# Performance work log

Measured on AMD Instinct MI355X. Metric: run time of the kernel, lower is better.

## Reference

```python
import jax, jax.numpy as jnp
import numpy as np

D_MODEL, D_K, D_V, H = 1024, 64, 64, 16
B, NQ, NK = 4, 1024, 1024
HID = D_MODEL // 2


def _dwg(x, W1, b1, W2, b2):
    # DynamicWeightGenerator: sigmoid(fc2(relu(fc1(x))))
    h = jax.nn.relu(jnp.einsum('bnd,hd->bnh', x, W1) + b1)
    return jax.nn.sigmoid(jnp.einsum('bnh,dh->bnd', h, W2) + b2)


def setup_inputs() -> dict:
    key = jax.random.key(0)
    ks = jax.random.split(key, 32)
    s = 0.02
    inp = {
        'queries': jax.random.normal(ks[0], (B, NQ, D_MODEL), jnp.float32),
        'keys': jax.random.normal(ks[1], (B, NK, D_MODEL), jnp.float32),
        'values': jax.random.normal(ks[2], (B, NK, D_MODEL), jnp.float32),
        'attention_mask': jax.random.randint(ks[3], (B, 1, NQ, NK), 0, 2) > 0,
        'attention_weights': jax.random.uniform(ks[4], (B, H, NQ, NK), jnp.float32),
        'memory': jax.random.normal(ks[5], (B, NK), jnp.float32),
        # projections (torch Linear convention: y = x @ W.T + b)
        'Wq': jax.random.normal(ks[6], (H * D_K, D_MODEL), jnp.float32) * s,
        'bq': jnp.zeros((H * D_K,), jnp.float32),
        'Wk': jax.random.normal(ks[7], (H * D_K, D_MODEL), jnp.float32) * s,
        'bk': jnp.zeros((H * D_K,), jnp.float32),
        'Wv': jax.random.normal(ks[8], (H * D_V, D_MODEL), jnp.float32) * s,
        'bv': jnp.zeros((H * D_V,), jnp.float32),
        'Wo': jax.random.normal(ks[9], (D_MODEL, H * D_V), jnp.float32) * s,
        'bo': jnp.zeros((D_MODEL,), jnp.float32),
        'Wmm': jax.random.normal(ks[10], (H * D_V, 1), jnp.float32) * s,
        'bmm': jnp.zeros((H * D_V,), jnp.float32),
    }
    for i, tag in enumerate(['q', 'k', 'v']):
        k0, k1 = ks[11 + 2 * i], ks[12 + 2 * i]
        inp[f'W1{tag}'] = jax.random.normal(k0, (HID, D_MODEL), jnp.float32) * s
        inp[f'b1{tag}'] = jnp.zeros((HID,), jnp.float32)
        inp[f'W2{tag}'] = jax.random.normal(k1, (D_MODEL, HID), jnp.float32) * s
        inp[f'b2{tag}'] = jnp.zeros((D_MODEL,), jnp.float32)
    return inp


def reference(queries, keys, values, attention_mask, attention_weights, memory,
              Wq, bq, Wk, bk, Wv, bv, Wo, bo, Wmm, bmm,
              W1q, b1q, W2q, b2q, W1k, b1k, W2k, b2k, W1v, b1v, W2v, b2v):
    b_s, nq = queries.shape[:2]
    nk = keys.shape[1]
    # dynamic elementwise gating of inputs
    q_in = queries * _dwg(queries, W1q, b1q, W2q, b2q)
    k_in = keys * _dwg(keys, W1k, b1k, W2k, b2k)
    v_in = values * _dwg(values, W1v, b1v, W2v, b2v)
    # projections -> (b, h, n, d)
    q = (jnp.einsum('bnd,ed->bne', q_in, Wq) + bq).reshape(b_s, nq, H, D_K).transpose(0, 2, 1, 3)
    k = (jnp.einsum('bnd,ed->bne', k_in, Wk) + bk).reshape(b_s, nk, H, D_K).transpose(0, 2, 1, 3)
    v = (jnp.einsum('bnd,ed->bne', v_in, Wv) + bv).reshape(b_s, nk, H, D_V).transpose(0, 2, 1, 3)
    # per-token memory factor: fc_mm(memory[..., None]) -> (b, h, nk, d_k)
    mm = (memory[..., None] * Wmm[:, 0] + bmm).reshape(b_s, nk, H, D_K).transpose(0, 2, 1, 3)
    att = jnp.einsum('bhqd,bhkd->bhqk', q, k * mm) / np.sqrt(D_K).astype(np.float32)
    att = att * attention_weights                         # custom scaling (slice [:nk] == full)
    att = jnp.where(attention_mask, -jnp.inf, att)        # masked_fill
    att = jax.nn.softmax(att, axis=-1)
    out = jnp.einsum('bhqk,bhkd->bhqd', att, v * mm)      # (b, h, nq, d_v)
    out = out.transpose(0, 2, 1, 3).reshape(b_s, nq, H * D_V)
    return jnp.einsum('bne,de->bnd', out, Wo) + bo
```

## Files before the change

### kernel.cpp

```cpp
#include <hip/hip_runtime.h>
#include <hip/hip_bf16.h>

#define BB    4
#define NN    1024
#define DM    1024
#define HH    16
#define HID   512
#define TT    (BB * NN)

typedef __attribute__((ext_vector_type(8))) short bf16x8;
typedef __attribute__((ext_vector_type(4))) float f32x4;

__device__ __forceinline__ ushort f2bfu(float f) {
    __hip_bfloat16 h = __float2bfloat16(f);
    return __builtin_bit_cast(ushort, h);
}

__device__ __forceinline__ float bfu2f(ushort u) {
    __hip_bfloat16 h = __builtin_bit_cast(__hip_bfloat16, u);
    return __bfloat162float(h);
}

__device__ __forceinline__ f32x4 mfma16(bf16x8 a, bf16x8 b, f32x4 c) {
    return __builtin_amdgcn_mfma_f32_16x16x32_bf16(a, b, c, 0, 0, 0);
}

__device__ __forceinline__ void gll16(const void* g, void* l) {
    __builtin_amdgcn_global_load_lds(
        (const __attribute__((address_space(1))) unsigned int*)g,
        (__attribute__((address_space(3))) unsigned int*)l, 16, 0, 0);
}

__global__ void detect_mask_kernel(const uint4* __restrict__ m,
                                   int n16, int* __restrict__ flags) {
    int stride = blockDim.x * gridDim.x;
    unsigned hi = 0, lo = 0;
    for (int i = blockIdx.x * blockDim.x + threadIdx.x; i < n16; i += stride) {
        uint4 v = m[i];
        unsigned o = v.x | v.y | v.z | v.w;
        lo |= o & 0xFFu;
        hi |= o & 0xFFFFFF00u;
    }
    if (hi) atomicOr(&flags[0], 1);
    if (lo) atomicOr(&flags[1], 1);
}

#define NSEG 13
struct CvtAll { const float* s[NSEG]; ushort* d[NSEG]; int bound[NSEG]; };

__global__ __launch_bounds__(256) void cvt_all(CvtAll a, int total) {
    int stride = blockDim.x * gridDim.x;
    for (int i = blockIdx.x * blockDim.x + threadIdx.x; i < total; i += stride) {
        const float* sp = a.s[0];
        ushort* dp = a.d[0];
        int base = 0;
        #pragma unroll
        for (int k = 1; k < NSEG; ++k) {
            bool ge = i >= a.bound[k - 1];
            sp = ge ? a.s[k] : sp;
            dp = ge ? a.d[k] : dp;
            base = ge ? a.bound[k - 1] : base;
        }
        int j = i - base;
        float4 v = ((const float4*)sp)[j];
        uint2 o;
        o.x = (unsigned)f2bfu(v.x) | ((unsigned)f2bfu(v.y) << 16);
        o.y = (unsigned)f2bfu(v.z) | ((unsigned)f2bfu(v.w) << 16);
        ((uint2*)dp)[j] = o;
    }
}

struct GB {
    const ushort* A[3]; const ushort* W[3];
    const float* bias[3]; void* C[3]; const ushort* X[3];
};

template <int EP, int NF>
__global__ __launch_bounds__(256) void gemm_bf16(
    GB gb, int M, int N, int K,
    const float* __restrict__ mem, const float* __restrict__ Wmm,
    const float* __restrict__ bmm)
{
    __shared__ __align__(16) ushort As[2][128 * 64];
    __shared__ __align__(16) ushort Bs[2][NF * 32 * 64];
    const int z = blockIdx.z;
    const ushort* A = gb.A[z];
    const ushort* W = gb.W[z];
    const float* bias = gb.bias[z];
    void* Cout = gb.C[z];
    const ushort* X = gb.X[z];

    const int tid = threadIdx.x;
    const int lane = tid & 63, w = tid >> 6;
    const int lc = lane & 15, lg = lane >> 4;
    const int m0 = blockIdx.x * 128, n0 = blockIdx.y * (NF * 32);
    const int wm = (w >> 1) * 64, wn = (w & 1) * (NF * 16);
    const int srow = lane >> 3, scol = 8 * ((lane & 7) ^ srow);
    const int swl = (lc & 7) << 3;

    f32x4 acc[4][NF];
    #pragma unroll
    for (int i = 0; i < 4; ++i)
        #pragma unroll
        for (int j = 0; j < NF; ++j)
            acc[i][j] = (f32x4){0.f, 0.f, 0.f, 0.f};

    auto stage = [&](int buf, int k0) {
        #pragma unroll
        for (int ci = 0; ci < 4; ++ci) {
            int c = w + ci * 4;
            gll16(&A[(size_t)(m0 + c * 8 + srow) * K + k0 + scol], &As[buf][c * 512]);
            if (c < NF * 4)
                gll16(&W[(size_t)(n0 + c * 8 + srow) * K + k0 + scol], &Bs[buf][c * 512]);
        }
    };

    stage(0, 0);
    stage(1, 64);
    const int nt = K / 64;

    for (int t = 0; t < nt; ++t) {
        const int cur = t & 1;
        if (t < nt - 1) {
            if constexpr (NF == 4) asm volatile("s_waitcnt vmcnt(8)" ::: "memory");
            else                   asm volatile("s_waitcnt vmcnt(6)" ::: "memory");
        } else {
            asm volatile("s_waitcnt vmcnt(0)" ::: "memory");
        }
        __builtin_amdgcn_sched_barrier(0);
        __builtin_amdgcn_s_barrier();

        bf16x8 af[4][2], bfr[NF][2];
        #pragma unroll
        for (int mi = 0; mi < 4; ++mi) {
            int row = wm + mi * 16 + lc;
            af[mi][0] = *(const bf16x8*)&As[cur][row * 64 + ((lg * 8) ^ swl)];
            af[mi][1] = *(const bf16x8*)&As[cur][row * 64 + ((32 + lg * 8) ^ swl)];
        }
        #pragma unroll
        for (int nj = 0; nj < NF; ++nj) {
            int row = wn + nj * 16 + lc;
            bfr[nj][0] = *(const bf16x8*)&Bs[cur][row * 64 + ((lg * 8) ^ swl)];
            bfr[nj][1] = *(const bf16x8*)&Bs[cur][row * 64 + ((32 + lg * 8) ^ swl)];
        }
        asm volatile("s_waitcnt lgkmcnt(0)" ::: "memory");
        __builtin_amdgcn_sched_barrier(0);
        __builtin_amdgcn_s_barrier();

        if (t + 2 < nt) stage(cur, (t + 2) * 64);

        #pragma unroll
        for (int mi = 0; mi < 4; ++mi)
            #pragma unroll
            for (int nj = 0; nj < NF; ++nj) {
                acc[mi][nj] = mfma16(af[mi][0], bfr[nj][0], acc[mi][nj]);
                acc[mi][nj] = mfma16(af[mi][1], bfr[nj][1], acc[mi][nj]);
            }
    }

    #pragma unroll
    for (int nj = 0; nj < NF; ++nj) {
        int e = n0 + wn + nj * 16 + lc;
        float bv = bias[e];
        float wmv = 0.f, bmv = 0.f;
        if (EP == 7) { wmv = Wmm[e]; bmv = bmm[e]; }
        #pragma unroll
        for (int mi = 0; mi < 4; ++mi) {
            int mbase = m0 + wm + mi * 16 + lg * 4;
            if (EP == 7 && z == 2) {
                ushort u[4];
                #pragma unroll
                for (int r = 0; r < 4; ++r) {
                    float v = (acc[mi][nj][r] + bv) * (mem[mbase + r] * wmv + bmv);
                    u[r] = f2bfu(v);
                }
                int bb = mbase >> 10, n = mbase & 1023;
                size_t off = ((size_t)(bb * HH + (e >> 6)) * 64 + (e & 63)) * NN + n;
                uint2 pk;
                pk.x = (unsigned)u[0] | ((unsigned)u[1] << 16);
                pk.y = (unsigned)u[2] | ((unsigned)u[3] << 16);
                *(uint2*)&((ushort*)Cout)[off] = pk;
            } else {
                #pragma unroll
                for (int r = 0; r < 4; ++r) {
                    int m = mbase + r;
                    float v = acc[mi][nj][r] + bv;
                    if (EP == 1) v = fmaxf(v, 0.f);
                    if (EP == 2) v = bfu2f(X[(size_t)m * N + e]) * (1.f / (1.f + __expf(-v)));
                    if (EP == 7) {
                        if (z == 0) v = v * 0.125f;
                        else        v = v * (mem[m] * wmv + bmv);
                    }
                    size_t off = (size_t)m * N + e;
                    if (EP == 4) ((float*)Cout)[off] = v;
                    else         ((ushort*)Cout)[off] = f2bfu(v);
                }
            }
        }
    }
}

__global__ __launch_bounds__(256) void attn_mfma(
    const ushort* __restrict__ qp, const ushort* __restrict__ kp,
    const ushort* __restrict__ vt, const float* __restrict__ aw,
    const void* __restrict__ maskp, const int* __restrict__ mflags,
    ushort* __restrict__ ob)
{
    __shared__ __align__(16) ushort Ks[2][64 * 64];
    __shared__ __align__(16) ushort Vs[2][64 * 64];
    __shared__ __align__(16) ushort Ps[64 * 64];
    const int tid = threadIdx.x, lane = tid & 63, w = tid >> 6;
    const int lc = lane & 15, lg = lane >> 4;
    const int bid = blockIdx.x;
    const int swz = (bid & 7) * 128 + (bid >> 3);
    const int qt = swz & 15, bh = swz >> 4;
    const int b = bh >> 4, h = bh & 15;
    const int q0 = qt * 64, wq = w * 16;
    const int mode = mflags[0] ? (mflags[1] ? 1 : 2) : 0;
    const int srow = lane >> 3, scol = 8 * ((lane & 7) ^ srow);
    const int swl = (lc & 7) << 3;

    const ushort* qrow = &qp[(size_t)(b * NN + q0 + wq + lc) * DM + h * 64];
    bf16x8 bq0 = *(const bf16x8*)&qrow[lg * 8];
    bf16x8 bq1 = *(const bf16x8*)&qrow[32 + lg * 8];

    f32x4 oacc[4];
    #pragma unroll
    for (int i = 0; i < 4; ++i) oacc[i] = (f32x4){0.f, 0.f, 0.f, 0.f};
    float psum = 0.f;
    const int q = q0 + wq + lc;
    const float* awrow = aw + ((size_t)bh * NN + q) * NN;
    const size_t mrowo = ((size_t)b * NN + q) * NN;

    float4 awA[4], awB[4];
    uint4 mk4A[4], mk4B[4];
    unsigned mk1A[4], mk1B[4];

    #pragma unroll
    for (int ci = 0; ci < 2; ++ci) {
        int c = w + ci * 4;
        gll16(&kp[(size_t)(b * NN + c * 8 + srow) * DM + h * 64 + scol], &Ks[0][c * 512]);
        gll16(&vt[((size_t)bh * 64 + c * 8 + srow) * NN + 0 + scol], &Vs[0][c * 512]);
    }
    #pragma unroll
    for (int mi = 0; mi < 4; ++mi)
        awA[mi] = *(const float4*)&awrow[mi * 16 + lg * 4];
    if (mode == 1) {
        #pragma unroll
        for (int mi = 0; mi < 4; ++mi)
            mk1A[mi] = *(const unsigned*)&((const unsigned char*)maskp)[mrowo + mi * 16 + lg * 4];
    } else {
        #pragma unroll
        for (int mi = 0; mi < 4; ++mi)
            mk4A[mi] = *(const uint4*)((const char*)maskp + 4 * (mrowo + mi * 16 + lg * 4));
    }
    asm volatile("s_waitcnt vmcnt(0)" ::: "memory");
    __builtin_amdgcn_sched_barrier(0);
    __builtin_amdgcn_s_barrier();

#define ATTN_BODY(T, AWC, MK4C, MK1C, AWN, MK4N, MK1N)                          \
    {                                                                           \
        const int cur = (T) & 1;                                                \
        if ((T) < 15) {                                                         \
            const int kn = ((T) + 1) * 64;                                      \
            _Pragma("unroll")                                                   \
            for (int ci = 0; ci < 2; ++ci) {                                    \
                int c = w + ci * 4;                                             \
                gll16(&kp[(size_t)(b * NN + kn + c * 8 + srow) * DM + h * 64 + scol], \
                      &Ks[cur ^ 1][c * 512]);                                   \
                gll16(&vt[((size_t)bh * 64 + c * 8 + srow) * NN + kn + scol],   \
                      &Vs[cur ^ 1][c * 512]);                                   \
            }                                                                   \
            __builtin_amdgcn_sched_barrier(0);                                  \
            _Pragma("unroll")                                                   \
            for (int mi = 0; mi < 4; ++mi)                                      \
                AWN[mi] = *(const float4*)&awrow[kn + mi * 16 + lg * 4];        \
            if (mode == 1) {                                                    \
                _Pragma("unroll")                                               \
                for (int mi = 0; mi < 4; ++mi)                                  \
                    MK1N[mi] = *(const unsigned*)&((const unsigned char*)maskp) \
                                   [mrowo + kn + mi * 16 + lg * 4];             \
            } else {                                                            \
                _Pragma("unroll")                                               \
                for (int mi = 0; mi < 4; ++mi)                                  \
                    MK4N[mi] = *(const uint4*)((const char*)maskp +             \
                                   4 * (mrowo + kn + mi * 16 + lg * 4));        \
            }                                                                   \
            __builtin_amdgcn_sched_barrier(0);                                  \
        }                                                                       \
                                                               \
        f32x4 sacc[4];                                                          \
        __builtin_amdgcn_s_setprio(1);                                          \
        _Pragma("unroll")                                                       \
        for (int mi = 0; mi < 4; ++mi) {                                        \
            int krow = mi * 16 + lc;                                            \
            bf16x8 a0 = *(const bf16x8*)&Ks[cur][krow * 64 + ((lg * 8) ^ swl)]; \
            bf16x8 a1 = *(const bf16x8*)&Ks[cur][krow * 64 + ((32 + lg * 8) ^ swl)]; \
            f32x4 s = (f32x4){0.f, 0.f, 0.f, 0.f};                              \
            s = mfma16(a0, bq0, s);                                             \
            s = mfma16(a1, bq1, s);                                             \
            sacc[mi] = s;                                                       \
        }                                                                       \
        __builtin_amdgcn_s_setprio(0);                                          \
                                 \
        _Pragma("unroll")                                                       \
        for (int mi = 0; mi < 4; ++mi) {                                        \
            unsigned mk[4];                                                     \
            if (mode == 1) {                                                    \
                mk[0] = MK1C[mi] & 0xffu;         mk[1] = (MK1C[mi] >> 8) & 0xffu;  \
                mk[2] = (MK1C[mi] >> 16) & 0xffu; mk[3] = (MK1C[mi] >> 24) & 0xffu; \
            } else if (mode == 0) {                                             \
                mk[0] = MK4C[mi].x; mk[1] = MK4C[mi].y;                         \
                mk[2] = MK4C[mi].z; mk[3] = MK4C[mi].w;                         \
            } else {                                                            \
                mk[0] = MK4C[mi].x != 0; mk[1] = MK4C[mi].y != 0;               \
                mk[2] = MK4C[mi].z != 0; mk[3] = MK4C[mi].w != 0;               \
            }                                                                   \
            const float aww[4] = {AWC[mi].x, AWC[mi].y, AWC[mi].z, AWC[mi].w};  \
            float pv[4];                                                        \
            _Pragma("unroll")                                                   \
            for (int r = 0; r < 4; ++r) {                                       \
                float sv = sacc[mi][r] * aww[r];                                \
                pv[r] = mk[r] ? 0.f : __expf(sv);                               \
                psum += pv[r];                                                  \
            }                                                                   \
            uint2 pk;                                                           \
            pk.x = (unsigned)f2bfu(pv[0]) | ((unsigned)f2bfu(pv[1]) << 16);     \
            pk.y = (unsigned)f2bfu(pv[2]) | ((unsigned)f2bfu(pv[3]) << 16);     \
            *(uint2*)&Ps[(wq + lc) * 64 + ((mi * 16 + lg * 4) ^ swl)] = pk;     \
        }                                                                       \
                                                                        \
        __builtin_amdgcn_s_setprio(1);                                          \
        _Pragma("unroll")                                                       \
        for (int kk = 0; kk < 2; ++kk) {                                        \
            bf16x8 pa = *(const bf16x8*)&Ps[(wq + lc) * 64 + ((kk * 32 + lg * 8) ^ swl)]; \
            _Pragma("unroll")                                                   \
            for (int nj = 0; nj < 4; ++nj) {                                    \
                bf16x8 vb = *(const bf16x8*)&Vs[cur][(nj * 16 + lc) * 64 + ((kk * 32 + lg * 8) ^ swl)]; \
                oacc[nj] = mfma16(pa, vb, oacc[nj]);                            \
            }                                                                   \
        }                                                                       \
        __builtin_amdgcn_s_setprio(0);                                          \
        if ((T) < 15) {                                                         \
            asm volatile("s_waitcnt vmcnt(0)" ::: "memory");                    \
            __builtin_amdgcn_sched_barrier(0);                                  \
            __builtin_amdgcn_s_barrier();                                       \
        }                                                                       \
    }

    for (int tt = 0; tt < 8; ++tt) {
        const int t0 = tt * 2, t1 = tt * 2 + 1;
        ATTN_BODY(t0, awA, mk4A, mk1A, awB, mk4B, mk1B);
        ATTN_BODY(t1, awB, mk4B, mk1B, awA, mk4A, mk1A);
    }
#undef ATTN_BODY

    psum += __shfl_xor(psum, 16);
    psum += __shfl_xor(psum, 32);
    float inv = 1.0f / psum;
    float invr[4];
    #pragma unroll
    for (int r = 0; r < 4; ++r)
        invr[r] = __shfl(inv, (lane & 48) | (lg * 4 + r));

    #pragma unroll
    for (int nj = 0; nj < 4; ++nj)
        #pragma unroll
        for (int r = 0; r < 4; ++r) {
            int qq = q0 + wq + lg * 4 + r;
            float v = oacc[nj][r] * invr[r];
            ob[(size_t)(b * NN + qq) * DM + h * 64 + nj * 16 + lc] = f2bfu(v);
        }
}

extern "C" void kernel_launch(void* const* d_in, const int* in_sizes, int n_in,
                              void* d_out, int out_size, void* d_ws, size_t ws_size,
                              hipStream_t stream) {
    const float* xin_f[3] = {(const float*)d_in[0], (const float*)d_in[1], (const float*)d_in[2]};
    const void*  maskp   = d_in[3];
    const float* aw      = (const float*)d_in[4];
    const float* memv    = (const float*)d_in[5];
    const float* Wp_f[3] = {(const float*)d_in[6], (const float*)d_in[8], (const float*)d_in[10]};
    const float* bp[3]   = {(const float*)d_in[7], (const float*)d_in[9], (const float*)d_in[11]};
    const float* Wo_f  = (const float*)d_in[12];  const float* bo  = (const float*)d_in[13];
    const float* Wmm = (const float*)d_in[14];    const float* bmm = (const float*)d_in[15];
    const float* W1f[3] = {(const float*)d_in[16], (const float*)d_in[20], (const float*)d_in[24]};
    const float* b1a[3] = {(const float*)d_in[17], (const float*)d_in[21], (const float*)d_in[25]};
    const float* W2f[3] = {(const float*)d_in[18], (const float*)d_in[22], (const float*)d_in[26]};
    const float* b2a[3] = {(const float*)d_in[19], (const float*)d_in[23], (const float*)d_in[27]};

    char* p = (char*)d_ws;
    auto alloc = [&](size_t bytes) { char* r = p; p += (bytes + 255) & ~(size_t)255; return r; };
    int*    mflags = (int*)alloc(256);
    ushort* xbf[3]; for (int t = 0; t < 3; ++t) xbf[t] = (ushort*)alloc((size_t)TT * DM * 2);
    ushort* Wpb[3]; for (int t = 0; t < 3; ++t) Wpb[t] = (ushort*)alloc((size_t)DM * DM * 2);
    ushort* Wob  = (ushort*)alloc((size_t)DM * DM * 2);
    ushort* W1b[3]; for (int t = 0; t < 3; ++t) W1b[t] = (ushort*)alloc((size_t)HID * DM * 2);
    ushort* W2b[3]; for (int t = 0; t < 3; ++t) W2b[t] = (ushort*)alloc((size_t)DM * HID * 2);
    ushort* hbuf[3]; for (int t = 0; t < 3; ++t) hbuf[t] = (ushort*)alloc((size_t)TT * HID * 2);
    ushort* xg[3];  for (int t = 0; t < 3; ++t) xg[t] = (ushort*)alloc((size_t)TT * DM * 2);
    ushort* qpb  = (ushort*)alloc((size_t)TT * DM * 2);
    ushort* ksb  = (ushort*)alloc((size_t)TT * DM * 2);
    ushort* vtb  = (ushort*)alloc((size_t)TT * DM * 2);
    ushort* obuf = (ushort*)alloc((size_t)TT * DM * 2);

    hipMemsetAsync(mflags, 0, 8, stream);
    detect_mask_kernel<<<256, 256, 0, stream>>>((const uint4*)maskp,
                                                BB * NN * NN / 16, mflags);

    {
        CvtAll a;
        const int S_IN = TT * DM / 4, S_W = DM * DM / 4, S_H = HID * DM / 4;
        int idx = 0, cum = 0;
        auto seg = [&](const float* s, ushort* d, int n) {
            a.s[idx] = s; a.d[idx] = d; cum += n; a.bound[idx] = cum; ++idx;
        };
        for (int t = 0; t < 3; ++t) seg(xin_f[t], xbf[t], S_IN);
        for (int t = 0; t < 3; ++t) seg(Wp_f[t], Wpb[t], S_W);
        seg(Wo_f, Wob, S_W);
        for (int t = 0; t < 3; ++t) seg(W1f[t], W1b[t], S_H);
        for (int t = 0; t < 3; ++t) seg(W2f[t], W2b[t], S_H);
        cvt_all<<<2048, 256, 0, stream>>>(a, cum);
    }

    const dim3 blk(256);
    GB g1 = {}, g2 = {}, g3 = {}, g4 = {};
    for (int t = 0; t < 3; ++t) {
        g1.A[t] = xbf[t];  g1.W[t] = W1b[t]; g1.bias[t] = b1a[t]; g1.C[t] = hbuf[t];
        g2.A[t] = hbuf[t]; g2.W[t] = W2b[t]; g2.bias[t] = b2a[t]; g2.C[t] = xg[t]; g2.X[t] = xbf[t];
        g3.A[t] = xg[t];   g3.W[t] = Wpb[t]; g3.bias[t] = bp[t];
    }
    g3.C[0] = qpb; g3.C[1] = ksb; g3.C[2] = vtb;
    g4.A[0] = obuf; g4.W[0] = Wob; g4.bias[0] = bo; g4.C[0] = d_out;

    gemm_bf16<1, 2><<<dim3(TT / 128, HID / 64, 3), blk, 0, stream>>>(g1, TT, HID, DM, nullptr, nullptr, nullptr);
    gemm_bf16<2, 2><<<dim3(TT / 128, DM / 64, 3), blk, 0, stream>>>(g2, TT, DM, HID, nullptr, nullptr, nullptr);
    gemm_bf16<7, 2><<<dim3(TT / 128, DM / 64, 3), blk, 0, stream>>>(g3, TT, DM, DM, memv, Wmm, bmm);

    attn_mfma<<<dim3(1024), blk, 0, stream>>>(qpb, ksb, vtb, aw,
                                              maskp, mflags, obuf);

    gemm_bf16<4, 2><<<dim3(TT / 128, DM / 64, 1), blk, 0, stream>>>(g4, TT, DM, DM, nullptr, nullptr, nullptr);
}
```

Baseline: 260.9 us.

## Fuse mask detection into conversion kernel and single-buffer attention K/V tiles

Merges the mask-detection kernel into the bf16 conversion kernel by giving detection its own extra blocks, which removes one kernel launch. Separately, the attention kernel drops double buffering of the K/V shared-memory tiles. The next tile is now loaded only after compute on the current one finishes, behind an extra barrier. This cuts LDS use, which may raise occupancy, but the K/V loads no longer overlap with the MFMA work.

```diff
diff --git a/kernel.cpp b/kernel.cpp
--- a/kernel.cpp
+++ b/kernel.cpp
@@ -31,42 +31,45 @@
         (__attribute__((address_space(3))) unsigned int*)l, 16, 0, 0);
 }
 
-__global__ void detect_mask_kernel(const uint4* __restrict__ m,
-                                   int n16, int* __restrict__ flags) {
-    int stride = blockDim.x * gridDim.x;
-    unsigned hi = 0, lo = 0;
-    for (int i = blockIdx.x * blockDim.x + threadIdx.x; i < n16; i += stride) {
-        uint4 v = m[i];
-        unsigned o = v.x | v.y | v.z | v.w;
-        lo |= o & 0xFFu;
-        hi |= o & 0xFFFFFF00u;
-    }
-    if (hi) atomicOr(&flags[0], 1);
-    if (lo) atomicOr(&flags[1], 1);
-}
-
 #define NSEG 13
 struct CvtAll { const float* s[NSEG]; ushort* d[NSEG]; int bound[NSEG]; };
 
-__global__ __launch_bounds__(256) void cvt_all(CvtAll a, int total) {
-    int stride = blockDim.x * gridDim.x;
-    for (int i = blockIdx.x * blockDim.x + threadIdx.x; i < total; i += stride) {
-        const float* sp = a.s[0];
-        ushort* dp = a.d[0];
-        int base = 0;
-        #pragma unroll
-        for (int k = 1; k < NSEG; ++k) {
-            bool ge = i >= a.bound[k - 1];
-            sp = ge ? a.s[k] : sp;
-            dp = ge ? a.d[k] : dp;
-            base = ge ? a.bound[k - 1] : base;
-        }
-        int j = i - base;
-        float4 v = ((const float4*)sp)[j];
-        uint2 o;
-        o.x = (unsigned)f2bfu(v.x) | ((unsigned)f2bfu(v.y) << 16);
-        o.y = (unsigned)f2bfu(v.z) | ((unsigned)f2bfu(v.w) << 16);
-        ((uint2*)dp)[j] = o;
+__global__ __launch_bounds__(256) void cvt_detect(
+    CvtAll a, int total, const uint4* __restrict__ m, int n16,
+    int* __restrict__ flags)
+{
+    if (blockIdx.x < 2048) {
+        int stride = 256 * 2048;
+        for (int i = blockIdx.x * 256 + threadIdx.x; i < total; i += stride) {
+            const float* sp = a.s[0];
+            ushort* dp = a.d[0];
+            int base = 0;
+            #pragma unroll
+            for (int k = 1; k < NSEG; ++k) {
+                bool ge = i >= a.bound[k - 1];
+                sp = ge ? a.s[k] : sp;
+                dp = ge ? a.d[k] : dp;
+                base = ge ? a.bound[k - 1] : base;
+            }
+            int j = i - base;
+            float4 v = ((const float4*)sp)[j];
+            uint2 o;
+            o.x = (unsigned)f2bfu(v.x) | ((unsigned)f2bfu(v.y) << 16);
+            o.y = (unsigned)f2bfu(v.z) | ((unsigned)f2bfu(v.w) << 16);
+            ((uint2*)dp)[j] = o;
+        }
+    } else {
+        int bid = blockIdx.x - 2048;
+        int stride = 256 * 256;
+        unsigned hi = 0, lo = 0;
+        for (int i = bid * 256 + threadIdx.x; i < n16; i += stride) {
+            uint4 v = m[i];
+            unsigned o = v.x | v.y | v.z | v.w;
+            lo |= o & 0xFFu;
+            hi |= o & 0xFFFFFF00u;
+        }
+        if (hi) atomicOr(&flags[0], 1);
+        if (lo) atomicOr(&flags[1], 1);
     }
 }
 
@@ -206,8 +209,8 @@
     const void* __restrict__ maskp, const int* __restrict__ mflags,
     ushort* __restrict__ ob)
 {
-    __shared__ __align__(16) ushort Ks[2][64 * 64];
-    __shared__ __align__(16) ushort Vs[2][64 * 64];
+    __shared__ __align__(16) ushort Ks[64 * 64];
+    __shared__ __align__(16) ushort Vs[64 * 64];
     __shared__ __align__(16) ushort Ps[64 * 64];
     const int tid = threadIdx.x, lane = tid & 63, w = tid >> 6;
     const int lc = lane & 15, lg = lane >> 4;
@@ -239,8 +242,8 @@
     #pragma unroll
     for (int ci = 0; ci < 2; ++ci) {
         int c = w + ci * 4;
-        gll16(&kp[(size_t)(b * NN + c * 8 + srow) * DM + h * 64 + scol], &Ks[0][c * 512]);
-        gll16(&vt[((size_t)bh * 64 + c * 8 + srow) * NN + 0 + scol], &Vs[0][c * 512]);
+        gll16(&kp[(size_t)(b * NN + c * 8 + srow) * DM + h * 64 + scol], &Ks[c * 512]);
+        gll16(&vt[((size_t)bh * 64 + c * 8 + srow) * NN + 0 + scol], &Vs[c * 512]);
     }
     #pragma unroll
     for (int mi = 0; mi < 4; ++mi)
@@ -260,18 +263,8 @@
 
 #define ATTN_BODY(T, AWC, MK4C, MK1C, AWN, MK4N, MK1N)                          \
     {                                                                           \
-        const int cur = (T) & 1;                                                \
-        if ((T) < 15) {                                                         \
+        if ((T) < 15) {                  \
             const int kn = ((T) + 1) * 64;                                      \
-            _Pragma("unroll")                                                   \
-            for (int ci = 0; ci < 2; ++ci) {                                    \
-                int c = w + ci * 4;                                             \
-                gll16(&kp[(size_t)(b * NN + kn + c * 8 + srow) * DM + h * 64 + scol], \
-                      &Ks[cur ^ 1][c * 512]);                                   \
-                gll16(&vt[((size_t)bh * 64 + c * 8 + srow) * NN + kn + scol],   \
-                      &Vs[cur ^ 1][c * 512]);                                   \
-            }                                                                   \
-            __builtin_amdgcn_sched_barrier(0);                                  \
             _Pragma("unroll")                                                   \
             for (int mi = 0; mi < 4; ++mi)                                      \
                 AWN[mi] = *(const float4*)&awrow[kn + mi * 16 + lg * 4];        \
@@ -294,8 +287,8 @@
         _Pragma("unroll")                                                       \
         for (int mi = 0; mi < 4; ++mi) {                                        \
             int krow = mi * 16 + lc;                                            \
-            bf16x8 a0 = *(const bf16x8*)&Ks[cur][krow * 64 + ((lg * 8) ^ swl)]; \
-            bf16x8 a1 = *(const bf16x8*)&Ks[cur][krow * 64 + ((32 + lg * 8) ^ swl)]; \
+            bf16x8 a0 = *(const bf16x8*)&Ks[krow * 64 + ((lg * 8) ^ swl)];      \
+            bf16x8 a1 = *(const bf16x8*)&Ks[krow * 64 + ((32 + lg * 8) ^ swl)]; \
             f32x4 s = (f32x4){0.f, 0.f, 0.f, 0.f};                              \
             s = mfma16(a0, bq0, s);                                             \
             s = mfma16(a1, bq1, s);                                             \
@@ -336,15 +329,25 @@
             bf16x8 pa = *(const bf16x8*)&Ps[(wq + lc) * 64 + ((kk * 32 + lg * 8) ^ swl)]; \
             _Pragma("unroll")                                                   \
             for (int nj = 0; nj < 4; ++nj) {                                    \
-                bf16x8 vb = *(const bf16x8*)&Vs[cur][(nj * 16 + lc) * 64 + ((kk * 32 + lg * 8) ^ swl)]; \
+                bf16x8 vb = *(const bf16x8*)&Vs[(nj * 16 + lc) * 64 + ((kk * 32 + lg * 8) ^ swl)]; \
                 oacc[nj] = mfma16(pa, vb, oacc[nj]);                            \
             }                                                                   \
         }                                                                       \
         __builtin_amdgcn_s_setprio(0);                                          \
         if ((T) < 15) {                                                         \
+            __builtin_amdgcn_s_barrier();         \
+            const int kn = ((T) + 1) * 64;                                      \
+            _Pragma("unroll")                                                   \
+            for (int ci = 0; ci < 2; ++ci) {       \
+                int c = w + ci * 4;                                             \
+                gll16(&kp[(size_t)(b * NN + kn + c * 8 + srow) * DM + h * 64 + scol], \
+                      &Ks[c * 512]);                                            \
+                gll16(&vt[((size_t)bh * 64 + c * 8 + srow) * NN + kn + scol],   \
+                      &Vs[c * 512]);                                            \
+            }                                                                   \
             asm volatile("s_waitcnt vmcnt(0)" ::: "memory");                    \
             __builtin_amdgcn_sched_barrier(0);                                  \
-            __builtin_amdgcn_s_barrier();                                       \
+            __builtin_amdgcn_s_barrier();                   \
         }                                                                       \
     }
 
@@ -405,8 +408,6 @@
     ushort* obuf = (ushort*)alloc((size_t)TT * DM * 2);
 
     hipMemsetAsync(mflags, 0, 8, stream);
-    detect_mask_kernel<<<256, 256, 0, stream>>>((const uint4*)maskp,
-                                                BB * NN * NN / 16, mflags);
 
     {
         CvtAll a;
@@ -420,7 +421,8 @@
         seg(Wo_f, Wob, S_W);
         for (int t = 0; t < 3; ++t) seg(W1f[t], W1b[t], S_H);
         for (int t = 0; t < 3; ++t) seg(W2f[t], W2b[t], S_H);
-        cvt_all<<<2048, 256, 0, stream>>>(a, cum);
+        cvt_detect<<<2304, 256, 0, stream>>>(a, cum, (const uint4*)maskp,
+                                             BB * NN * NN / 16, mflags);
     }
 
     const dim3 blk(256);
```

Measured after the change: 263.9 us. About the same (+1.1%).
